# Kernel optimization log

Measured on AMD Instinct MI355X. Metric: run time of the kernel, lower is better.

Reference implementation:

```python
import jax, jax.numpy as jnp
import numpy as np

N_NODES = 100000
N_EDGES = 1600000
IN_FEATS, HIDDEN, N_CLASSES = 128, 64, 16


def setup_inputs() -> dict:
    key = jax.random.key(0)
    ks = jax.random.split(key, 10)
    feats = jax.random.normal(ks[0], (N_NODES, IN_FEATS), dtype=jnp.float32)
    src = jax.random.randint(ks[1], (N_EDGES,), 0, N_NODES, dtype=jnp.int32)
    dst = jax.random.randint(ks[2], (N_EDGES,), 0, N_NODES, dtype=jnp.int32)
    def glorot(k, fan_in, fan_out):
        lim = np.sqrt(6.0 / (fan_in + fan_out)).astype(np.float32)
        return jax.random.uniform(k, (fan_in, fan_out), jnp.float32, -lim, lim)
    return {
        "features": feats, "src": src, "dst": dst,
        "W0": glorot(ks[3], IN_FEATS, HIDDEN), "b0": jnp.zeros((HIDDEN,), jnp.float32),
        "W1": glorot(ks[4], HIDDEN, HIDDEN), "b1": jnp.zeros((HIDDEN,), jnp.float32),
        "W2": glorot(ks[5], HIDDEN, N_CLASSES), "b2": jnp.zeros((N_CLASSES,), jnp.float32),
    }


def _graph_conv(src, dst, x, W, b, act):
    # DGL GraphConv, norm='both': out = D_in^{-1/2} A (D_out^{-1/2} x) W + b
    n = x.shape[0]
    ones = jnp.ones((src.shape[0],), x.dtype)
    deg_out = jnp.clip(jax.ops.segment_sum(ones, src, num_segments=n), 1.0)
    deg_in = jnp.clip(jax.ops.segment_sum(ones, dst, num_segments=n), 1.0)
    # DGL applies W first when in_dim > out_dim (same math, less edge traffic)
    pre = x.shape[1] > W.shape[1]
    h = x @ W if pre else x
    h = h * jax.lax.rsqrt(deg_out)[:, None]
    agg = jax.ops.segment_sum(h[src], dst, num_segments=n)  # [N, d]
    agg = agg * jax.lax.rsqrt(deg_in)[:, None]
    out = (agg if pre else agg @ W) + b
    return act(out) if act is not None else out


def reference(features, src, dst, W0, b0, W1, b1, W2, b2):
    relu = jax.nn.relu
    h = _graph_conv(src, dst, features, W0, b0, relu)
    h = _graph_conv(src, dst, h, W1, b1, relu)        # dropout p=0.0 -> identity
    h = _graph_conv(src, dst, h, W2, b2, None)
    return h
```

## Files before the change

kernel.cpp:

```cpp
#include <hip/hip_runtime.h>

#define NN 100000
#define NE 1600000
#define NBUCK 782
#define PCHUNK 8192
#define HISTB 256
#define NREP 8
#define STAGE_CAP 12288

struct alignas(8) US4 { unsigned short x, y, z, w; };

__device__ __forceinline__ float bfu(unsigned int hw) { return __uint_as_float(hw << 16); }
__device__ __forceinline__ unsigned short f2bf(float f) {
    unsigned int u = __float_as_uint(f);
    return (unsigned short)((u + 0x7fffu + ((u >> 16) & 1u)) >> 16);
}


__global__ __launch_bounds__(256) void k_hist(const int* __restrict__ src,
                                              const int* __restrict__ dst,
                                              int* __restrict__ bcnt8_d,
                                              int* __restrict__ bcnt8_s) {
    __shared__ int hd[NBUCK], hs[NBUCK];
    int tid = threadIdx.x;
    for (int i = tid; i < NBUCK; i += 256) { hd[i] = 0; hs[i] = 0; }
    __syncthreads();
    int* md = bcnt8_d + (size_t)(blockIdx.x & (NREP - 1)) * NBUCK;
    int* ms = bcnt8_s + (size_t)(blockIdx.x & (NREP - 1)) * NBUCK;
    int stride = gridDim.x * 256;
    for (int e = blockIdx.x * 256 + tid; e < NE; e += stride) {
        atomicAdd(&hd[dst[e] >> 7], 1);
        atomicAdd(&hs[src[e] >> 7], 1);
    }
    __syncthreads();
    for (int i = tid; i < NBUCK; i += 256) {
        if (hd[i]) atomicAdd(&md[i], hd[i]);
        if (hs[i]) atomicAdd(&ms[i], hs[i]);
    }
}

__global__ __launch_bounds__(1024) void k_bscan(const int* __restrict__ bcnt8_d,
                                                const int* __restrict__ bcnt8_s,
                                                int* __restrict__ base_d,
                                                int* __restrict__ base_s,
                                                unsigned long long* __restrict__ cur64,
                                                unsigned short* __restrict__ A,
                                                unsigned short* __restrict__ B,
                                                unsigned short* __restrict__ C16,
                                                int* __restrict__ EBg) {
    int t = threadIdx.x;
    if (blockIdx.x == 1) {
        if (t < 64) {
            A[(size_t)NN * 64 + t] = 0;
            B[(size_t)NN * 64 + t] = 0;
        }
        if (t < 16) {
            C16[(size_t)NN * 16 + t] = 0;
            EBg[NE + t] = NN;
        }
        return;
    }
    __shared__ int tmp[1024];
    int v = 0;
    if (t < NBUCK)
#pragma unroll
        for (int c = 0; c < NREP; ++c) v += bcnt8_d[c * NBUCK + t];
    tmp[t] = v;
    __syncthreads();
    for (int off = 1; off < 1024; off <<= 1) {
        int u = (t >= off) ? tmp[t - off] : 0;
        __syncthreads();
        tmp[t] += u;
        __syncthreads();
    }
    int excl_d = tmp[t] - v;
    if (t < NBUCK) base_d[t] = excl_d;
    if (t == 0) base_d[NBUCK] = NE;
    __syncthreads();
    v = 0;
    if (t < NBUCK)
#pragma unroll
        for (int c = 0; c < NREP; ++c) v += bcnt8_s[c * NBUCK + t];
    tmp[t] = v;
    __syncthreads();
    for (int off = 1; off < 1024; off <<= 1) {
        int u = (t >= off) ? tmp[t - off] : 0;
        __syncthreads();
        tmp[t] += u;
        __syncthreads();
    }
    int excl_s = tmp[t] - v;
    if (t < NBUCK) {
        base_s[t] = excl_s;
        cur64[t] = (unsigned long long)(unsigned)excl_d |
                   ((unsigned long long)(unsigned)excl_s << 32);
    }
    if (t == 0) base_s[NBUCK] = NE;
}

__global__ __launch_bounds__(512) void k_pairs(const int* __restrict__ src,
                                               const int* __restrict__ dst,
                                               unsigned long long* __restrict__ cur64,
                                               int* __restrict__ E2d,
                                               unsigned char* __restrict__ E2s) {
    __shared__ int hist_d[NBUCK], gbase_d[NBUCK], hist_s[NBUCK], gbase_s[NBUCK];
    int tid = threadIdx.x;
    for (int i = tid; i < NBUCK; i += 512) { hist_d[i] = 0; hist_s[i] = 0; }
    __syncthreads();
    int base = blockIdx.x * PCHUNK;
#pragma unroll
    for (int i = 0; i < PCHUNK / 512; ++i) {
        int e = base + i * 512 + tid;
        if (e < NE) {
            atomicAdd(&hist_d[dst[e] >> 7], 1);
            atomicAdd(&hist_s[src[e] >> 7], 1);
        }
    }
    __syncthreads();
    int rot = (int)((blockIdx.x * 191u) % NBUCK);
    for (int ii = tid; ii < NBUCK; ii += 512) {
        int i = ii + rot;
        if (i >= NBUCK) i -= NBUCK;
        int hd = hist_d[i], hs = hist_s[i];
        if (hd | hs) {
            unsigned long long r = atomicAdd(
                &cur64[i], (unsigned long long)(unsigned)hd |
                               ((unsigned long long)(unsigned)hs << 32));
            gbase_d[i] = (int)(r & 0xffffffffu);
            gbase_s[i] = (int)(r >> 32);
        }
        hist_d[i] = 0;
        hist_s[i] = 0;
    }
    __syncthreads();
#pragma unroll
    for (int i = 0; i < PCHUNK / 512; ++i) {
        int e = base + i * 512 + tid;
        if (e < NE) {
            int s = src[e], d = dst[e];
            int bd = d >> 7;
            int pd = atomicAdd(&hist_d[bd], 1);
            E2d[gbase_d[bd] + pd] = (s << 7) | (d & 127);
            int bs = s >> 7;
            int ps = atomicAdd(&hist_s[bs], 1);
            E2s[gbase_s[bs] + ps] = (unsigned char)(s & 127);
        }
    }
}

__global__ __launch_bounds__(256) void k_nodes(int* __restrict__ EB,
                                               const int* __restrict__ base_d,
                                               const unsigned char* __restrict__ E2s,
                                               const int* __restrict__ base_s,
                                               int* __restrict__ rowdesc,
                                               float* __restrict__ r_in,
                                               float* __restrict__ r_out) {
    __shared__ int cnt[128], cur[128];
    __shared__ int stage[STAGE_CAP];
    int tid = threadIdx.x;
    int b = blockIdx.x;
    if (b >= NBUCK) {
        b -= NBUCK;
        int base = base_s[b], end = base_s[b + 1];
        if (tid < 128) cnt[tid] = 0;
        __syncthreads();
        for (int i = base + tid; i < end; i += 256) atomicAdd(&cnt[E2s[i]], 1);
        __syncthreads();
        if (tid < 128) {
            int node = b * 128 + tid;
            if (node < NN) r_out[node] = rsqrtf((float)max(cnt[tid], 1));
        }
        return;
    }
    int base = base_d[b], end = base_d[b + 1];
    int m = min(end - base, STAGE_CAP);
    if (tid < 128) cnt[tid] = 0;
    __syncthreads();
    for (int i = tid; i < m; i += 256) {
        int e = EB[base + i];
        stage[i] = e;
        atomicAdd(&cnt[e & 127], 1);
    }
    __syncthreads();
    int v = (tid < 128) ? cnt[tid] : 0;
    for (int off = 1; off < 128; off <<= 1) {
        int u = (tid >= off && tid < 128) ? cnt[tid - off] : 0;
        __syncthreads();
        if (tid < 128) cnt[tid] += u;
        __syncthreads();
    }
    if (tid < 128) {
        int excl = cnt[tid] - v;
        cur[tid] = excl;
        int node = b * 128 + tid;
        if (node < NN) {
            rowdesc[node] = ((base + excl) << 9) | min(v, 511);
            r_in[node] = rsqrtf((float)max(v, 1));
        }
    }
    __syncthreads();
    for (int i = tid; i < m; i += 256) {
        int e = stage[i];
        int pos = atomicAdd(&cur[e & 127], 1);
        EB[base + pos] = e >> 7;
    }
}


__global__ __launch_bounds__(256) void k_gemm0(const float* __restrict__ x,
                                               const float* __restrict__ W0,
                                               const float* __restrict__ r_out,
                                               unsigned short* __restrict__ A) {
    __shared__ float xl[64 * 129];
    __shared__ float wl[64 * 64];
    int tid = threadIdx.x;
    int m0 = blockIdx.x * 64;
#pragma unroll
    for (int i = 0; i < 8; ++i) {
        int idx = i * 256 + tid;
        int m = idx >> 5, kc = idx & 31;
        int gm = min(m0 + m, NN - 1);
        float4 v = *(const float4*)&x[(size_t)gm * 128 + kc * 4];
        float* p = &xl[m * 129 + kc * 4];
        p[0] = v.x; p[1] = v.y; p[2] = v.z; p[3] = v.w;
    }
    int tn = tid & 15, tm = tid >> 4;
    float acc[4][4] = {};
    const float4* W4 = (const float4*)W0;
    float4* wl4 = (float4*)wl;
    for (int h = 0; h < 2; ++h) {
        __syncthreads();
#pragma unroll
        for (int i = 0; i < 4; ++i) wl4[i * 256 + tid] = W4[h * 1024 + i * 256 + tid];
        __syncthreads();
#pragma unroll 4
        for (int k = 0; k < 64; ++k) {
            int kk = h * 64 + k;
            float4 wv = *(const float4*)&wl[k * 64 + tn * 4];
            float xv[4];
#pragma unroll
            for (int i = 0; i < 4; ++i) xv[i] = xl[(tm * 4 + i) * 129 + kk];
#pragma unroll
            for (int i = 0; i < 4; ++i) {
                acc[i][0] = fmaf(xv[i], wv.x, acc[i][0]);
                acc[i][1] = fmaf(xv[i], wv.y, acc[i][1]);
                acc[i][2] = fmaf(xv[i], wv.z, acc[i][2]);
                acc[i][3] = fmaf(xv[i], wv.w, acc[i][3]);
            }
        }
    }
#pragma unroll
    for (int i = 0; i < 4; ++i) {
        int m = m0 + tm * 4 + i;
        if (m < NN) {
            float ro = r_out[m];
            US4 o = {f2bf(acc[i][0] * ro), f2bf(acc[i][1] * ro),
                     f2bf(acc[i][2] * ro), f2bf(acc[i][3] * ro)};
            *(US4*)&A[(size_t)m * 64 + tn * 4] = o;
        }
    }
}

__global__ __launch_bounds__(256) void k_mlp(const unsigned short* __restrict__ G,
                                             const float* __restrict__ W1,
                                             const float* __restrict__ b1,
                                             const float* __restrict__ W2,
                                             const float* __restrict__ r_out,
                                             unsigned short* __restrict__ C16) {
    __shared__ float gl[64 * 65];
    __shared__ float w1l[64 * 64];
    __shared__ float w2l[64 * 16];
    int tid = threadIdx.x;
    int m0 = blockIdx.x * 64;
#pragma unroll
    for (int i = 0; i < 2; ++i) {
        int idx = i * 256 + tid;
        int m = idx >> 3, c8 = idx & 7;
        int gm = min(m0 + m, NN - 1);
        uint4 u = *(const uint4*)&G[(size_t)gm * 64 + c8 * 8];
        float* p = &gl[m * 65 + c8 * 8];
        p[0] = bfu(u.x & 0xffffu); p[1] = bfu(u.x >> 16);
        p[2] = bfu(u.y & 0xffffu); p[3] = bfu(u.y >> 16);
        p[4] = bfu(u.z & 0xffffu); p[5] = bfu(u.z >> 16);
        p[6] = bfu(u.w & 0xffffu); p[7] = bfu(u.w >> 16);
    }
    float4* w1l4 = (float4*)w1l;
    const float4* W1_4 = (const float4*)W1;
#pragma unroll
    for (int i = 0; i < 4; ++i) w1l4[i * 256 + tid] = W1_4[i * 256 + tid];
    ((float4*)w2l)[tid] = ((const float4*)W2)[tid];
    __syncthreads();
    int tn = tid & 15, tm = tid >> 4;
    float acc[4][4] = {};
#pragma unroll 4
    for (int k = 0; k < 64; ++k) {
        float4 wv = *(const float4*)&w1l[k * 64 + tn * 4];
        float xv[4];
#pragma unroll
        for (int i = 0; i < 4; ++i) xv[i] = gl[(tm * 4 + i) * 65 + k];
#pragma unroll
        for (int i = 0; i < 4; ++i) {
            acc[i][0] = fmaf(xv[i], wv.x, acc[i][0]);
            acc[i][1] = fmaf(xv[i], wv.y, acc[i][1]);
            acc[i][2] = fmaf(xv[i], wv.z, acc[i][2]);
            acc[i][3] = fmaf(xv[i], wv.w, acc[i][3]);
        }
    }
    float4 bb = *(const float4*)&b1[tn * 4];
    __syncthreads();
#pragma unroll
    for (int i = 0; i < 4; ++i) {
        gl[(tm * 4 + i) * 65 + tn * 4 + 0] = fmaxf(acc[i][0] + bb.x, 0.f);
        gl[(tm * 4 + i) * 65 + tn * 4 + 1] = fmaxf(acc[i][1] + bb.y, 0.f);
        gl[(tm * 4 + i) * 65 + tn * 4 + 2] = fmaxf(acc[i][2] + bb.z, 0.f);
        gl[(tm * 4 + i) * 65 + tn * 4 + 3] = fmaxf(acc[i][3] + bb.w, 0.f);
    }
    __syncthreads();
    int m = tid >> 2, n0 = (tid & 3) * 4;
    float a2[4] = {};
#pragma unroll 8
    for (int k = 0; k < 64; ++k) {
        float zv = gl[m * 65 + k];
        float4 wv = *(const float4*)&w2l[k * 16 + n0];
        a2[0] = fmaf(zv, wv.x, a2[0]);
        a2[1] = fmaf(zv, wv.y, a2[1]);
        a2[2] = fmaf(zv, wv.z, a2[2]);
        a2[3] = fmaf(zv, wv.w, a2[3]);
    }
    int node = m0 + m;
    if (node < NN) {
        float ro = r_out[node];
        US4 o = {f2bf(a2[0] * ro), f2bf(a2[1] * ro), f2bf(a2[2] * ro), f2bf(a2[3] * ro)};
        *(US4*)&C16[(size_t)node * 16 + n0] = o;
    }
}


template <int MODE>
__global__ __launch_bounds__(256) void k_gb64(const int* __restrict__ rowdesc,
                                              const int* __restrict__ csr,
                                              const unsigned short* __restrict__ h,
                                              const float* __restrict__ r_in,
                                              const float* __restrict__ r_out,
                                              const float* __restrict__ bias,
                                              unsigned short* __restrict__ o16) {
    int tid = threadIdx.x;
    int wave = tid >> 6, lane = tid & 63;
    int n0 = (blockIdx.x * 4 + wave) * 2, n1 = n0 + 1;
    int rdA = rowdesc[n0], rdB = rowdesc[n1];
    int jbA = rdA >> 9, degA = rdA & 511;
    int jbB = rdB >> 9, degB = rdB & 511;
    int itn = max((degA + 7) >> 3, (degB + 7) >> 3);
    int g = lane >> 3, f8 = lane & 7;
    const int* cA = csr + jbA + g;
    const int* cB = csr + jbB + g;
    const unsigned short* hp = h + f8 * 8;
    float aA[8] = {}, aB[8] = {};
    for (int it = 0; it < itn; it += 2) {
        int s0 = it * 8 + g, s1 = s0 + 8;
        int eA0 = cA[it * 8];
        int eA1 = cA[it * 8 + 8];
        int eB0 = cB[it * 8];
        int eB1 = cB[it * 8 + 8];
        eA0 = (s0 < degA) ? eA0 : NN;
        eA1 = (s1 < degA) ? eA1 : NN;
        eB0 = (s0 < degB) ? eB0 : NN;
        eB1 = (s1 < degB) ? eB1 : NN;
        uint4 u0 = *(const uint4*)(hp + (size_t)eA0 * 64);
        uint4 u1 = *(const uint4*)(hp + (size_t)eA1 * 64);
        uint4 u2 = *(const uint4*)(hp + (size_t)eB0 * 64);
        uint4 u3 = *(const uint4*)(hp + (size_t)eB1 * 64);
        aA[0] += bfu(u0.x & 0xffffu); aA[1] += bfu(u0.x >> 16);
        aA[2] += bfu(u0.y & 0xffffu); aA[3] += bfu(u0.y >> 16);
        aA[4] += bfu(u0.z & 0xffffu); aA[5] += bfu(u0.z >> 16);
        aA[6] += bfu(u0.w & 0xffffu); aA[7] += bfu(u0.w >> 16);
        aA[0] += bfu(u1.x & 0xffffu); aA[1] += bfu(u1.x >> 16);
        aA[2] += bfu(u1.y & 0xffffu); aA[3] += bfu(u1.y >> 16);
        aA[4] += bfu(u1.z & 0xffffu); aA[5] += bfu(u1.z >> 16);
        aA[6] += bfu(u1.w & 0xffffu); aA[7] += bfu(u1.w >> 16);
        aB[0] += bfu(u2.x & 0xffffu); aB[1] += bfu(u2.x >> 16);
        aB[2] += bfu(u2.y & 0xffffu); aB[3] += bfu(u2.y >> 16);
        aB[4] += bfu(u2.z & 0xffffu); aB[5] += bfu(u2.z >> 16);
        aB[6] += bfu(u2.w & 0xffffu); aB[7] += bfu(u2.w >> 16);
        aB[0] += bfu(u3.x & 0xffffu); aB[1] += bfu(u3.x >> 16);
        aB[2] += bfu(u3.y & 0xffffu); aB[3] += bfu(u3.y >> 16);
        aB[4] += bfu(u3.z & 0xffffu); aB[5] += bfu(u3.z >> 16);
        aB[6] += bfu(u3.w & 0xffffu); aB[7] += bfu(u3.w >> 16);
    }
#pragma unroll
    for (int m = 8; m <= 32; m <<= 1) {
#pragma unroll
        for (int k = 0; k < 8; ++k) {
            aA[k] += __shfl_xor(aA[k], m);
            aB[k] += __shfl_xor(aB[k], m);
        }
    }
    if (g < 2) {
        int nw = g ? n1 : n0;
        float o[8];
#pragma unroll
        for (int k = 0; k < 8; ++k) o[k] = g ? aB[k] : aA[k];
        float ri = r_in[nw];
        unsigned short ov[8];
        if (MODE == 0) {
            float ro = r_out[nw];
            float4 bA = *(const float4*)&bias[f8 * 8];
            float4 bB = *(const float4*)&bias[f8 * 8 + 4];
            float bb[8] = {bA.x, bA.y, bA.z, bA.w, bB.x, bB.y, bB.z, bB.w};
#pragma unroll
            for (int k = 0; k < 8; ++k)
                ov[k] = f2bf(fmaxf(fmaf(o[k], ri, bb[k]), 0.f) * ro);
        } else {
#pragma unroll
            for (int k = 0; k < 8; ++k) ov[k] = f2bf(o[k] * ri);
        }
        uint4 ow;
        ow.x = (unsigned)ov[0] | ((unsigned)ov[1] << 16);
        ow.y = (unsigned)ov[2] | ((unsigned)ov[3] << 16);
        ow.z = (unsigned)ov[4] | ((unsigned)ov[5] << 16);
        ow.w = (unsigned)ov[6] | ((unsigned)ov[7] << 16);
        *(uint4*)&o16[(size_t)nw * 64 + f8 * 8] = ow;
    }
}

__global__ __launch_bounds__(256) void k_gb16(const int* __restrict__ rowdesc,
                                              const int* __restrict__ csr,
                                              const unsigned short* __restrict__ C16,
                                              const float* __restrict__ r_in,
                                              const float* __restrict__ b2,
                                              float* __restrict__ out) {
    int tid = threadIdx.x;
    int wave = tid >> 6, lane = tid & 63;
    int n0 = (blockIdx.x * 4 + wave) * 2, n1 = n0 + 1;
    int rdA = rowdesc[n0], rdB = rowdesc[n1];
    int jbA = rdA >> 9, degA = rdA & 511;
    int jbB = rdB >> 9, degB = rdB & 511;
    int itn = max((degA + 7) >> 3, (degB + 7) >> 3);
    int g = lane >> 3, p = lane & 7;
    const int* cA = csr + jbA + g;
    const int* cB = csr + jbB + g;
    const unsigned short* cp = C16 + p * 2;
    float a0A = 0.f, a1A = 0.f, a0B = 0.f, a1B = 0.f;
    for (int it = 0; it < itn; it += 2) {
        int s0 = it * 8 + g, s1 = s0 + 8;
        int eA0 = cA[it * 8];
        int eA1 = cA[it * 8 + 8];
        int eB0 = cB[it * 8];
        int eB1 = cB[it * 8 + 8];
        eA0 = (s0 < degA) ? eA0 : NN;
        eA1 = (s1 < degA) ? eA1 : NN;
        eB0 = (s0 < degB) ? eB0 : NN;
        eB1 = (s1 < degB) ? eB1 : NN;
        unsigned u0 = *(const unsigned*)(cp + (size_t)eA0 * 16);
        unsigned u1 = *(const unsigned*)(cp + (size_t)eA1 * 16);
        unsigned u2 = *(const unsigned*)(cp + (size_t)eB0 * 16);
        unsigned u3 = *(const unsigned*)(cp + (size_t)eB1 * 16);
        a0A += bfu(u0 & 0xffffu); a1A += bfu(u0 >> 16);
        a0A += bfu(u1 & 0xffffu); a1A += bfu(u1 >> 16);
        a0B += bfu(u2 & 0xffffu); a1B += bfu(u2 >> 16);
        a0B += bfu(u3 & 0xffffu); a1B += bfu(u3 >> 16);
    }
#pragma unroll
    for (int m = 8; m <= 32; m <<= 1) {
        a0A += __shfl_xor(a0A, m);
        a1A += __shfl_xor(a1A, m);
        a0B += __shfl_xor(a0B, m);
        a1B += __shfl_xor(a1B, m);
    }
    if (g < 2) {
        int nw = g ? n1 : n0;
        float x0 = g ? a0B : a0A;
        float x1 = g ? a1B : a1A;
        float ri = r_in[nw];
        float2 bb = *(const float2*)&b2[p * 2];
        float2 o;
        o.x = fmaf(x0, ri, bb.x);
        o.y = fmaf(x1, ri, bb.y);
        *(float2*)&out[(size_t)nw * 16 + p * 2] = o;
    }
}

extern "C" void kernel_launch(void* const* d_in, const int* in_sizes, int n_in,
                              void* d_out, int out_size, void* d_ws, size_t ws_size,
                              hipStream_t stream) {
    const float* feats = (const float*)d_in[0];
    const int* src = (const int*)d_in[1];
    const int* dst = (const int*)d_in[2];
    const float* W0 = (const float*)d_in[3];
    const float* b0 = (const float*)d_in[4];
    const float* W1 = (const float*)d_in[5];
    const float* b1 = (const float*)d_in[6];
    const float* W2 = (const float*)d_in[7];
    const float* b2 = (const float*)d_in[8];
    float* out = (float*)d_out;

    float* ws = (float*)d_ws;
    float* r_out = ws;
    float* r_in = ws + NN;
    int* rowdesc = (int*)(ws + 2 * NN);
    int* EB = (int*)(ws + 3 * NN);
    unsigned char* E2s = (unsigned char*)(ws + 3 * NN + NE + 16);
    float* R1 = ws + 3 * NN + NE + 16 + NE / 4;
    float* R2 = R1 + (size_t)32 * (NN + 1);
    float* Creg = R2 + (size_t)32 * (NN + 1);
    int* base_d = (int*)(Creg + (size_t)8 * (NN + 1));
    int* base_s = base_d + NBUCK + 1;
    int* cur_raw = base_s + NBUCK + 1;
    unsigned long long* cur64 =
        (unsigned long long*)(cur_raw + (((size_t)(cur_raw - (int*)ws)) & 1));
    int* bcnt8_d = (int*)(cur64 + NBUCK);
    int* bcnt8_s = bcnt8_d + NREP * NBUCK;

    unsigned short* A = (unsigned short*)R1;
    unsigned short* G = A;
    unsigned short* B = (unsigned short*)R2;
    unsigned short* C16 = (unsigned short*)Creg;

    hipMemsetAsync(bcnt8_d, 0, 2 * NREP * NBUCK * sizeof(int), stream);
    k_hist<<<HISTB, 256, 0, stream>>>(src, dst, bcnt8_d, bcnt8_s);
    k_bscan<<<2, 1024, 0, stream>>>(bcnt8_d, bcnt8_s, base_d, base_s, cur64,
                                    A, B, C16, EB);
    k_pairs<<<(NE + PCHUNK - 1) / PCHUNK, 512, 0, stream>>>(src, dst, cur64, EB, E2s);
    k_nodes<<<2 * NBUCK, 256, 0, stream>>>(EB, base_d, E2s, base_s, rowdesc, r_in, r_out);

    k_gemm0<<<(NN + 63) / 64, 256, 0, stream>>>(feats, W0, r_out, A);
    k_gb64<0><<<NN / 8, 256, 0, stream>>>(rowdesc, EB, A, r_in, r_out, b0, B);

    k_gb64<1><<<NN / 8, 256, 0, stream>>>(rowdesc, EB, B, r_in, r_out, b0, G);
    k_mlp<<<(NN + 63) / 64, 256, 0, stream>>>(G, W1, b1, W2, r_out, C16);

    k_gb16<<<NN / 8, 256, 0, stream>>>(rowdesc, EB, C16, r_in, b2, out);
}
```

Baseline: 334.5 us.

## Fuse all graph-conv stages into one persistent kernel with grid barriers

Replaces the chain of separate kernels (histogram, scan, pair scatter, node build, GEMM, three gathers, MLP) with a single persistent kernel of 512 blocks of 512 threads. Stages are separated by a hierarchical software grid barrier that uses atomic counters in workspace. Work in each stage is spread over the fixed grid with grid-stride loops. The aim is to remove per-launch overhead and idle gaps between the many short kernels. In exchange it depends on all blocks being co-resident, loses per-stage launch-shape tuning, and shares one union of shared memory across stages, which could limit occupancy.

```diff
diff --git a/kernel.cpp b/kernel.cpp
--- a/kernel.cpp
+++ b/kernel.cpp
@@ -3,8 +3,10 @@
 #define NN 100000
 #define NE 1600000
 #define NBUCK 782
+#define NB 512
+#define NT 512
 #define PCHUNK 8192
-#define HISTB 256
+#define NPB 196
 #define NREP 8
 #define STAGE_CAP 12288
 
@@ -16,467 +18,479 @@
     return (unsigned short)((u + 0x7fffu + ((u >> 16) & 1u)) >> 16);
 }
 
-
-__global__ __launch_bounds__(256) void k_hist(const int* __restrict__ src,
-                                              const int* __restrict__ dst,
-                                              int* __restrict__ bcnt8_d,
-                                              int* __restrict__ bcnt8_s) {
-    __shared__ int hd[NBUCK], hs[NBUCK];
+__device__ __forceinline__ void gbar(int* bars, int idx) {
+    __syncthreads();
+    if (threadIdx.x == 0) {
+        __threadfence();
+        int* base = bars + idx * 16;
+        int g = (int)(blockIdx.x & 7);
+        if (atomicAdd(&base[g], 1) == (NB / 8) - 1) atomicAdd(&base[8], 1);
+        while (__hip_atomic_load(&base[8], __ATOMIC_RELAXED,
+                                 __HIP_MEMORY_SCOPE_AGENT) < 8) {
+            __builtin_amdgcn_s_sleep(2);
+        }
+        __threadfence();
+    }
+    __syncthreads();
+}
+
+template <int MODE>
+__device__ __forceinline__ void gb64_phase(int bid, int tid,
+                                           const int* __restrict__ rowdesc,
+                                           const int* __restrict__ csr,
+                                           const unsigned short* __restrict__ h,
+                                           const float* __restrict__ r_in,
+                                           const float* __restrict__ r_out,
+                                           const float* __restrict__ bias,
+                                           unsigned short* __restrict__ o16) {
+    int wave = tid >> 6, lane = tid & 63;
+    int g = lane >> 3, f8 = lane & 7;
+    const unsigned short* hp = h + f8 * 8;
+    for (int u = bid; u < NN / 16; u += NB) {
+        int n0 = (u * 8 + wave) * 2, n1 = n0 + 1;
+        int rdA = rowdesc[n0], rdB = rowdesc[n1];
+        int jbA = rdA >> 9, degA = rdA & 511;
+        int jbB = rdB >> 9, degB = rdB & 511;
+        int itn = max((degA + 7) >> 3, (degB + 7) >> 3);
+        const int* cA = csr + jbA + g;
+        const int* cB = csr + jbB + g;
+        float aA[8] = {}, aB[8] = {};
+        for (int it = 0; it < itn; it += 2) {
+            int s0 = it * 8 + g, s1 = s0 + 8;
+            int eA0 = cA[it * 8];
+            int eA1 = cA[it * 8 + 8];
+            int eB0 = cB[it * 8];
+            int eB1 = cB[it * 8 + 8];
+            eA0 = (s0 < degA) ? eA0 : NN;
+            eA1 = (s1 < degA) ? eA1 : NN;
+            eB0 = (s0 < degB) ? eB0 : NN;
+            eB1 = (s1 < degB) ? eB1 : NN;
+            uint4 u0 = *(const uint4*)(hp + (size_t)eA0 * 64);
+            uint4 u1 = *(const uint4*)(hp + (size_t)eA1 * 64);
+            uint4 u2 = *(const uint4*)(hp + (size_t)eB0 * 64);
+            uint4 u3 = *(const uint4*)(hp + (size_t)eB1 * 64);
+            aA[0] += bfu(u0.x & 0xffffu); aA[1] += bfu(u0.x >> 16);
+            aA[2] += bfu(u0.y & 0xffffu); aA[3] += bfu(u0.y >> 16);
+            aA[4] += bfu(u0.z & 0xffffu); aA[5] += bfu(u0.z >> 16);
+            aA[6] += bfu(u0.w & 0xffffu); aA[7] += bfu(u0.w >> 16);
+            aA[0] += bfu(u1.x & 0xffffu); aA[1] += bfu(u1.x >> 16);
+            aA[2] += bfu(u1.y & 0xffffu); aA[3] += bfu(u1.y >> 16);
+            aA[4] += bfu(u1.z & 0xffffu); aA[5] += bfu(u1.z >> 16);
+            aA[6] += bfu(u1.w & 0xffffu); aA[7] += bfu(u1.w >> 16);
+            aB[0] += bfu(u2.x & 0xffffu); aB[1] += bfu(u2.x >> 16);
+            aB[2] += bfu(u2.y & 0xffffu); aB[3] += bfu(u2.y >> 16);
+            aB[4] += bfu(u2.z & 0xffffu); aB[5] += bfu(u2.z >> 16);
+            aB[6] += bfu(u2.w & 0xffffu); aB[7] += bfu(u2.w >> 16);
+            aB[0] += bfu(u3.x & 0xffffu); aB[1] += bfu(u3.x >> 16);
+            aB[2] += bfu(u3.y & 0xffffu); aB[3] += bfu(u3.y >> 16);
+            aB[4] += bfu(u3.z & 0xffffu); aB[5] += bfu(u3.z >> 16);
+            aB[6] += bfu(u3.w & 0xffffu); aB[7] += bfu(u3.w >> 16);
+        }
+#pragma unroll
+        for (int m = 8; m <= 32; m <<= 1) {
+#pragma unroll
+            for (int k = 0; k < 8; ++k) {
+                aA[k] += __shfl_xor(aA[k], m);
+                aB[k] += __shfl_xor(aB[k], m);
+            }
+        }
+        if (g < 2) {
+            int nw = g ? n1 : n0;
+            float o[8];
+#pragma unroll
+            for (int k = 0; k < 8; ++k) o[k] = g ? aB[k] : aA[k];
+            float ri = r_in[nw];
+            unsigned short ov[8];
+            if (MODE == 0) {
+                float ro = r_out[nw];
+                float4 bA = *(const float4*)&bias[f8 * 8];
+                float4 bB = *(const float4*)&bias[f8 * 8 + 4];
+                float bb[8] = {bA.x, bA.y, bA.z, bA.w, bB.x, bB.y, bB.z, bB.w};
+#pragma unroll
+                for (int k = 0; k < 8; ++k)
+                    ov[k] = f2bf(fmaxf(fmaf(o[k], ri, bb[k]), 0.f) * ro);
+            } else {
+#pragma unroll
+                for (int k = 0; k < 8; ++k) ov[k] = f2bf(o[k] * ri);
+            }
+            uint4 ow;
+            ow.x = (unsigned)ov[0] | ((unsigned)ov[1] << 16);
+            ow.y = (unsigned)ov[2] | ((unsigned)ov[3] << 16);
+            ow.z = (unsigned)ov[4] | ((unsigned)ov[5] << 16);
+            ow.w = (unsigned)ov[6] | ((unsigned)ov[7] << 16);
+            *(uint4*)&o16[(size_t)nw * 64 + f8 * 8] = ow;
+        }
+    }
+}
+
+struct SmemT {
+    union {
+        struct { int hd[NBUCK]; int hs[NBUCK]; } hist;
+        struct { int psum[NT]; } scan;
+        struct { int hist_d[NBUCK], gbase_d[NBUCK], hist_s[NBUCK], gbase_s[NBUCK]; } pairs;
+        struct { int cnt[128], cur[128]; int stage[STAGE_CAP]; } nodes;
+        struct { float xl[128 * 65]; float wl[64 * 64]; } gemm;
+        struct { float gl[128 * 65]; float w1l[64 * 64]; float w2l[64 * 16]; } mlp;
+    };
+};
+
+__global__ __launch_bounds__(NT, 4) void k_fused(
+    const float* __restrict__ x, const int* __restrict__ src,
+    const int* __restrict__ dst, const float* __restrict__ W0,
+    const float* __restrict__ b0, const float* __restrict__ W1,
+    const float* __restrict__ b1, const float* __restrict__ W2,
+    const float* __restrict__ b2, float* __restrict__ out,
+    float* __restrict__ r_out, float* __restrict__ r_in,
+    int* __restrict__ rowdesc, int* __restrict__ EB,
+    unsigned char* __restrict__ E2s, int* __restrict__ base_d,
+    int* __restrict__ base_s, unsigned long long* __restrict__ cur64,
+    int* __restrict__ bcnt8_d, int* __restrict__ bcnt8_s,
+    int* __restrict__ bars, unsigned short* __restrict__ A,
+    unsigned short* __restrict__ B, unsigned short* __restrict__ C16) {
+    __shared__ SmemT sm;
     int tid = threadIdx.x;
-    for (int i = tid; i < NBUCK; i += 256) { hd[i] = 0; hs[i] = 0; }
-    __syncthreads();
-    int* md = bcnt8_d + (size_t)(blockIdx.x & (NREP - 1)) * NBUCK;
-    int* ms = bcnt8_s + (size_t)(blockIdx.x & (NREP - 1)) * NBUCK;
-    int stride = gridDim.x * 256;
-    for (int e = blockIdx.x * 256 + tid; e < NE; e += stride) {
-        atomicAdd(&hd[dst[e] >> 7], 1);
-        atomicAdd(&hs[src[e] >> 7], 1);
-    }
-    __syncthreads();
-    for (int i = tid; i < NBUCK; i += 256) {
-        if (hd[i]) atomicAdd(&md[i], hd[i]);
-        if (hs[i]) atomicAdd(&ms[i], hs[i]);
-    }
-}
-
-__global__ __launch_bounds__(1024) void k_bscan(const int* __restrict__ bcnt8_d,
-                                                const int* __restrict__ bcnt8_s,
-                                                int* __restrict__ base_d,
-                                                int* __restrict__ base_s,
-                                                unsigned long long* __restrict__ cur64,
-                                                unsigned short* __restrict__ A,
-                                                unsigned short* __restrict__ B,
-                                                unsigned short* __restrict__ C16,
-                                                int* __restrict__ EBg) {
-    int t = threadIdx.x;
-    if (blockIdx.x == 1) {
-        if (t < 64) {
-            A[(size_t)NN * 64 + t] = 0;
-            B[(size_t)NN * 64 + t] = 0;
-        }
-        if (t < 16) {
-            C16[(size_t)NN * 16 + t] = 0;
-            EBg[NE + t] = NN;
-        }
-        return;
-    }
-    __shared__ int tmp[1024];
-    int v = 0;
-    if (t < NBUCK)
-#pragma unroll
-        for (int c = 0; c < NREP; ++c) v += bcnt8_d[c * NBUCK + t];
-    tmp[t] = v;
-    __syncthreads();
-    for (int off = 1; off < 1024; off <<= 1) {
-        int u = (t >= off) ? tmp[t - off] : 0;
+    int bid = blockIdx.x;
+
+    {
+        int tot = 2 * NREP * NBUCK;
+        for (int i = bid * NT + tid; i < tot; i += NB * NT) bcnt8_d[i] = 0;
+        if (bid == 0) {
+            if (tid < 64) {
+                A[(size_t)NN * 64 + tid] = 0;
+                B[(size_t)NN * 64 + tid] = 0;
+            }
+            if (tid < 16) {
+                C16[(size_t)NN * 16 + tid] = 0;
+                EB[NE + tid] = NN;
+            }
+        }
+    }
+    gbar(bars, 0);
+
+    {
+        for (int i = tid; i < NBUCK; i += NT) { sm.hist.hd[i] = 0; sm.hist.hs[i] = 0; }
         __syncthreads();
-        tmp[t] += u;
+        int* md = bcnt8_d + (size_t)(bid & (NREP - 1)) * NBUCK;
+        int* ms = bcnt8_s + (size_t)(bid & (NREP - 1)) * NBUCK;
+        for (int e = bid * NT + tid; e < NE; e += NB * NT) {
+            atomicAdd(&sm.hist.hd[dst[e] >> 7], 1);
+            atomicAdd(&sm.hist.hs[src[e] >> 7], 1);
+        }
         __syncthreads();
-    }
-    int excl_d = tmp[t] - v;
-    if (t < NBUCK) base_d[t] = excl_d;
-    if (t == 0) base_d[NBUCK] = NE;
-    __syncthreads();
-    v = 0;
-    if (t < NBUCK)
-#pragma unroll
-        for (int c = 0; c < NREP; ++c) v += bcnt8_s[c * NBUCK + t];
-    tmp[t] = v;
-    __syncthreads();
-    for (int off = 1; off < 1024; off <<= 1) {
-        int u = (t >= off) ? tmp[t - off] : 0;
+        for (int i = tid; i < NBUCK; i += NT) {
+            if (sm.hist.hd[i]) atomicAdd(&md[i], sm.hist.hd[i]);
+            if (sm.hist.hs[i]) atomicAdd(&ms[i], sm.hist.hs[i]);
+        }
+    }
+    gbar(bars, 1);
+
+    if (bid == 0) {
+        for (int side = 0; side < 2; ++side) {
+            const int* bc = side ? bcnt8_s : bcnt8_d;
+            int* base = side ? base_s : base_d;
+            int b0i = 2 * tid, b1i = 2 * tid + 1;
+            int s0 = 0, s1 = 0;
+            if (b0i < NBUCK)
+#pragma unroll
+                for (int c = 0; c < NREP; ++c) s0 += bc[c * NBUCK + b0i];
+            if (b1i < NBUCK)
+#pragma unroll
+                for (int c = 0; c < NREP; ++c) s1 += bc[c * NBUCK + b1i];
+            int tot = s0 + s1;
+            sm.scan.psum[tid] = tot;
+            __syncthreads();
+            for (int off = 1; off < NT; off <<= 1) {
+                int u = (tid >= off) ? sm.scan.psum[tid - off] : 0;
+                __syncthreads();
+                sm.scan.psum[tid] += u;
+                __syncthreads();
+            }
+            int excl = sm.scan.psum[tid] - tot;
+            if (b0i < NBUCK) base[b0i] = excl;
+            if (b1i < NBUCK) base[b1i] = excl + s0;
+            if (tid == 0) base[NBUCK] = NE;
+            __syncthreads();
+        }
+        for (int b = tid; b < NBUCK; b += NT)
+            cur64[b] = (unsigned long long)(unsigned)base_d[b] |
+                       ((unsigned long long)(unsigned)base_s[b] << 32);
+    }
+    gbar(bars, 2);
+
+    if (bid < NPB) {
+        for (int i = tid; i < NBUCK; i += NT) { sm.pairs.hist_d[i] = 0; sm.pairs.hist_s[i] = 0; }
         __syncthreads();
-        tmp[t] += u;
+        int base = bid * PCHUNK;
+#pragma unroll
+        for (int i = 0; i < PCHUNK / NT; ++i) {
+            int e = base + i * NT + tid;
+            if (e < NE) {
+                atomicAdd(&sm.pairs.hist_d[dst[e] >> 7], 1);
+                atomicAdd(&sm.pairs.hist_s[src[e] >> 7], 1);
+            }
+        }
         __syncthreads();
-    }
-    int excl_s = tmp[t] - v;
-    if (t < NBUCK) {
-        base_s[t] = excl_s;
-        cur64[t] = (unsigned long long)(unsigned)excl_d |
-                   ((unsigned long long)(unsigned)excl_s << 32);
-    }
-    if (t == 0) base_s[NBUCK] = NE;
-}
-
-__global__ __launch_bounds__(512) void k_pairs(const int* __restrict__ src,
-                                               const int* __restrict__ dst,
-                                               unsigned long long* __restrict__ cur64,
-                                               int* __restrict__ E2d,
-                                               unsigned char* __restrict__ E2s) {
-    __shared__ int hist_d[NBUCK], gbase_d[NBUCK], hist_s[NBUCK], gbase_s[NBUCK];
-    int tid = threadIdx.x;
-    for (int i = tid; i < NBUCK; i += 512) { hist_d[i] = 0; hist_s[i] = 0; }
-    __syncthreads();
-    int base = blockIdx.x * PCHUNK;
-#pragma unroll
-    for (int i = 0; i < PCHUNK / 512; ++i) {
-        int e = base + i * 512 + tid;
-        if (e < NE) {
-            atomicAdd(&hist_d[dst[e] >> 7], 1);
-            atomicAdd(&hist_s[src[e] >> 7], 1);
-        }
-    }
-    __syncthreads();
-    int rot = (int)((blockIdx.x * 191u) % NBUCK);
-    for (int ii = tid; ii < NBUCK; ii += 512) {
-        int i = ii + rot;
-        if (i >= NBUCK) i -= NBUCK;
-        int hd = hist_d[i], hs = hist_s[i];
-        if (hd | hs) {
-            unsigned long long r = atomicAdd(
-                &cur64[i], (unsigned long long)(unsigned)hd |
-                               ((unsigned long long)(unsigned)hs << 32));
-            gbase_d[i] = (int)(r & 0xffffffffu);
-            gbase_s[i] = (int)(r >> 32);
-        }
-        hist_d[i] = 0;
-        hist_s[i] = 0;
-    }
-    __syncthreads();
-#pragma unroll
-    for (int i = 0; i < PCHUNK / 512; ++i) {
-        int e = base + i * 512 + tid;
-        if (e < NE) {
-            int s = src[e], d = dst[e];
-            int bd = d >> 7;
-            int pd = atomicAdd(&hist_d[bd], 1);
-            E2d[gbase_d[bd] + pd] = (s << 7) | (d & 127);
-            int bs = s >> 7;
-            int ps = atomicAdd(&hist_s[bs], 1);
-            E2s[gbase_s[bs] + ps] = (unsigned char)(s & 127);
-        }
-    }
-}
-
-__global__ __launch_bounds__(256) void k_nodes(int* __restrict__ EB,
-                                               const int* __restrict__ base_d,
-                                               const unsigned char* __restrict__ E2s,
-                                               const int* __restrict__ base_s,
-                                               int* __restrict__ rowdesc,
-                                               float* __restrict__ r_in,
-                                               float* __restrict__ r_out) {
-    __shared__ int cnt[128], cur[128];
-    __shared__ int stage[STAGE_CAP];
-    int tid = threadIdx.x;
-    int b = blockIdx.x;
-    if (b >= NBUCK) {
-        b -= NBUCK;
-        int base = base_s[b], end = base_s[b + 1];
-        if (tid < 128) cnt[tid] = 0;
+        int rot = (int)((bid * 191u) % NBUCK);
+        for (int ii = tid; ii < NBUCK; ii += NT) {
+            int i = ii + rot;
+            if (i >= NBUCK) i -= NBUCK;
+            int hd = sm.pairs.hist_d[i], hs = sm.pairs.hist_s[i];
+            if (hd | hs) {
+                unsigned long long r = atomicAdd(
+                    &cur64[i], (unsigned long long)(unsigned)hd |
+                                   ((unsigned long long)(unsigned)hs << 32));
+                sm.pairs.gbase_d[i] = (int)(r & 0xffffffffu);
+                sm.pairs.gbase_s[i] = (int)(r >> 32);
+            }
+            sm.pairs.hist_d[i] = 0;
+            sm.pairs.hist_s[i] = 0;
+        }
         __syncthreads();
-        for (int i = base + tid; i < end; i += 256) atomicAdd(&cnt[E2s[i]], 1);
+#pragma unroll
+        for (int i = 0; i < PCHUNK / NT; ++i) {
+            int e = base + i * NT + tid;
+            if (e < NE) {
+                int s = src[e], d = dst[e];
+                int bd = d >> 7;
+                int pd = atomicAdd(&sm.pairs.hist_d[bd], 1);
+                EB[sm.pairs.gbase_d[bd] + pd] = (s << 7) | (d & 127);
+                int bs = s >> 7;
+                int ps = atomicAdd(&sm.pairs.hist_s[bs], 1);
+                E2s[sm.pairs.gbase_s[bs] + ps] = (unsigned char)(s & 127);
+            }
+        }
+    }
+    gbar(bars, 3);
+
+    for (int bb = bid; bb < 2 * NBUCK; bb += NB) {
         __syncthreads();
-        if (tid < 128) {
-            int node = b * 128 + tid;
-            if (node < NN) r_out[node] = rsqrtf((float)max(cnt[tid], 1));
-        }
-        return;
-    }
-    int base = base_d[b], end = base_d[b + 1];
-    int m = min(end - base, STAGE_CAP);
-    if (tid < 128) cnt[tid] = 0;
-    __syncthreads();
-    for (int i = tid; i < m; i += 256) {
-        int e = EB[base + i];
-        stage[i] = e;
-        atomicAdd(&cnt[e & 127], 1);
-    }
-    __syncthreads();
-    int v = (tid < 128) ? cnt[tid] : 0;
-    for (int off = 1; off < 128; off <<= 1) {
-        int u = (tid >= off && tid < 128) ? cnt[tid - off] : 0;
-        __syncthreads();
-        if (tid < 128) cnt[tid] += u;
-        __syncthreads();
-    }
-    if (tid < 128) {
-        int excl = cnt[tid] - v;
-        cur[tid] = excl;
-        int node = b * 128 + tid;
-        if (node < NN) {
-            rowdesc[node] = ((base + excl) << 9) | min(v, 511);
-            r_in[node] = rsqrtf((float)max(v, 1));
-        }
-    }
-    __syncthreads();
-    for (int i = tid; i < m; i += 256) {
-        int e = stage[i];
-        int pos = atomicAdd(&cur[e & 127], 1);
-        EB[base + pos] = e >> 7;
-    }
-}
-
-
-__global__ __launch_bounds__(256) void k_gemm0(const float* __restrict__ x,
-                                               const float* __restrict__ W0,
-                                               const float* __restrict__ r_out,
-                                               unsigned short* __restrict__ A) {
-    __shared__ float xl[64 * 129];
-    __shared__ float wl[64 * 64];
-    int tid = threadIdx.x;
-    int m0 = blockIdx.x * 64;
-#pragma unroll
-    for (int i = 0; i < 8; ++i) {
-        int idx = i * 256 + tid;
-        int m = idx >> 5, kc = idx & 31;
-        int gm = min(m0 + m, NN - 1);
-        float4 v = *(const float4*)&x[(size_t)gm * 128 + kc * 4];
-        float* p = &xl[m * 129 + kc * 4];
-        p[0] = v.x; p[1] = v.y; p[2] = v.z; p[3] = v.w;
-    }
-    int tn = tid & 15, tm = tid >> 4;
-    float acc[4][4] = {};
-    const float4* W4 = (const float4*)W0;
-    float4* wl4 = (float4*)wl;
-    for (int h = 0; h < 2; ++h) {
-        __syncthreads();
-#pragma unroll
-        for (int i = 0; i < 4; ++i) wl4[i * 256 + tid] = W4[h * 1024 + i * 256 + tid];
-        __syncthreads();
+        if (bb >= NBUCK) {
+            int b = bb - NBUCK;
+            int base = base_s[b], end = base_s[b + 1];
+            if (tid < 128) sm.nodes.cnt[tid] = 0;
+            __syncthreads();
+            for (int i = base + tid; i < end; i += NT) atomicAdd(&sm.nodes.cnt[E2s[i]], 1);
+            __syncthreads();
+            if (tid < 128) {
+                int node = b * 128 + tid;
+                if (node < NN) r_out[node] = rsqrtf((float)max(sm.nodes.cnt[tid], 1));
+            }
+        } else {
+            int b = bb;
+            int base = base_d[b], end = base_d[b + 1];
+            int m = min(end - base, STAGE_CAP);
+            if (tid < 128) sm.nodes.cnt[tid] = 0;
+            __syncthreads();
+            for (int i = tid; i < m; i += NT) {
+                int e = EB[base + i];
+                sm.nodes.stage[i] = e;
+                atomicAdd(&sm.nodes.cnt[e & 127], 1);
+            }
+            __syncthreads();
+            int v = (tid < 128) ? sm.nodes.cnt[tid] : 0;
+            for (int off = 1; off < 128; off <<= 1) {
+                int u = (tid >= off && tid < 128) ? sm.nodes.cnt[tid - off] : 0;
+                __syncthreads();
+                if (tid < 128) sm.nodes.cnt[tid] += u;
+                __syncthreads();
+            }
+            if (tid < 128) {
+                int excl = sm.nodes.cnt[tid] - v;
+                sm.nodes.cur[tid] = excl;
+                int node = b * 128 + tid;
+                if (node < NN) {
+                    rowdesc[node] = ((base + excl) << 9) | min(v, 511);
+                    r_in[node] = rsqrtf((float)max(v, 1));
+                }
+            }
+            __syncthreads();
+            for (int i = tid; i < m; i += NT) {
+                int e = sm.nodes.stage[i];
+                int pos = atomicAdd(&sm.nodes.cur[e & 127], 1);
+                EB[base + pos] = e >> 7;
+            }
+        }
+    }
+    gbar(bars, 4);
+
+    {
+        int tn = tid & 15, tm = tid >> 4;
+        const float4* W4 = (const float4*)W0;
+        float4* wl4 = (float4*)sm.gemm.wl;
+        for (int tile = bid; tile < (NN + 127) / 128; tile += NB) {
+            int m0 = tile * 128;
+            float acc[4][4] = {};
+            for (int h = 0; h < 2; ++h) {
+                __syncthreads();
+#pragma unroll
+                for (int i = 0; i < 4; ++i) {
+                    int idx = i * NT + tid;
+                    int m = idx >> 4, kc = idx & 15;
+                    int gm = min(m0 + m, NN - 1);
+                    float4 v = *(const float4*)&x[(size_t)gm * 128 + h * 64 + kc * 4];
+                    float* p = &sm.gemm.xl[m * 65 + kc * 4];
+                    p[0] = v.x; p[1] = v.y; p[2] = v.z; p[3] = v.w;
+                }
+#pragma unroll
+                for (int i = 0; i < 2; ++i) wl4[i * NT + tid] = W4[h * 1024 + i * NT + tid];
+                __syncthreads();
 #pragma unroll 4
-        for (int k = 0; k < 64; ++k) {
-            int kk = h * 64 + k;
-            float4 wv = *(const float4*)&wl[k * 64 + tn * 4];
-            float xv[4];
-#pragma unroll
-            for (int i = 0; i < 4; ++i) xv[i] = xl[(tm * 4 + i) * 129 + kk];
+                for (int k = 0; k < 64; ++k) {
+                    float4 wv = *(const float4*)&sm.gemm.wl[k * 64 + tn * 4];
+                    float xv[4];
+#pragma unroll
+                    for (int i = 0; i < 4; ++i) xv[i] = sm.gemm.xl[(tm * 4 + i) * 65 + k];
+#pragma unroll
+                    for (int i = 0; i < 4; ++i) {
+                        acc[i][0] = fmaf(xv[i], wv.x, acc[i][0]);
+                        acc[i][1] = fmaf(xv[i], wv.y, acc[i][1]);
+                        acc[i][2] = fmaf(xv[i], wv.z, acc[i][2]);
+                        acc[i][3] = fmaf(xv[i], wv.w, acc[i][3]);
+                    }
+                }
+            }
 #pragma unroll
             for (int i = 0; i < 4; ++i) {
-                acc[i][0] = fmaf(xv[i], wv.x, acc[i][0]);
-                acc[i][1] = fmaf(xv[i], wv.y, acc[i][1]);
-                acc[i][2] = fmaf(xv[i], wv.z, acc[i][2]);
-                acc[i][3] = fmaf(xv[i], wv.w, acc[i][3]);
-            }
-        }
-    }
-#pragma unroll
-    for (int i = 0; i < 4; ++i) {
-        int m = m0 + tm * 4 + i;
-        if (m < NN) {
-            float ro = r_out[m];
-            US4 o = {f2bf(acc[i][0] * ro), f2bf(acc[i][1] * ro),
-                     f2bf(acc[i][2] * ro), f2bf(acc[i][3] * ro)};
-            *(US4*)&A[(size_t)m * 64 + tn * 4] = o;
-        }
-    }
-}
-
-__global__ __launch_bounds__(256) void k_mlp(const unsigned short* __restrict__ G,
-                                             const float* __restrict__ W1,
-                                             const float* __restrict__ b1,
-                                             const float* __restrict__ W2,
-                                             const float* __restrict__ r_out,
-                                             unsigned short* __restrict__ C16) {
-    __shared__ float gl[64 * 65];
-    __shared__ float w1l[64 * 64];
-    __shared__ float w2l[64 * 16];
-    int tid = threadIdx.x;
-    int m0 = blockIdx.x * 64;
-#pragma unroll
-    for (int i = 0; i < 2; ++i) {
-        int idx = i * 256 + tid;
-        int m = idx >> 3, c8 = idx & 7;
-        int gm = min(m0 + m, NN - 1);
-        uint4 u = *(const uint4*)&G[(size_t)gm * 64 + c8 * 8];
-        float* p = &gl[m * 65 + c8 * 8];
-        p[0] = bfu(u.x & 0xffffu); p[1] = bfu(u.x >> 16);
-        p[2] = bfu(u.y & 0xffffu); p[3] = bfu(u.y >> 16);
-        p[4] = bfu(u.z & 0xffffu); p[5] = bfu(u.z >> 16);
-        p[6] = bfu(u.w & 0xffffu); p[7] = bfu(u.w >> 16);
-    }
-    float4* w1l4 = (float4*)w1l;
-    const float4* W1_4 = (const float4*)W1;
-#pragma unroll
-    for (int i = 0; i < 4; ++i) w1l4[i * 256 + tid] = W1_4[i * 256 + tid];
-    ((float4*)w2l)[tid] = ((const float4*)W2)[tid];
-    __syncthreads();
-    int tn = tid & 15, tm = tid >> 4;
-    float acc[4][4] = {};
+                int m = m0 + tm * 4 + i;
+                if (m < NN) {
+                    float ro = r_out[m];
+                    US4 o = {f2bf(acc[i][0] * ro), f2bf(acc[i][1] * ro),
+                             f2bf(acc[i][2] * ro), f2bf(acc[i][3] * ro)};
+                    *(US4*)&A[(size_t)m * 64 + tn * 4] = o;
+                }
+            }
+        }
+    }
+    gbar(bars, 5);
+
+    gb64_phase<0>(bid, tid, rowdesc, EB, A, r_in, r_out, b0, B);
+    gbar(bars, 6);
+
+    gb64_phase<1>(bid, tid, rowdesc, EB, B, r_in, r_out, b0, A);
+    gbar(bars, 7);
+
+    {
+        const unsigned short* G = A;
+        int tn = tid & 15, tm = tid >> 4;
+        float4* w1l4 = (float4*)sm.mlp.w1l;
+        const float4* W1_4 = (const float4*)W1;
+        for (int tile = bid; tile < (NN + 127) / 128; tile += NB) {
+            int m0 = tile * 128;
+            __syncthreads();
+#pragma unroll
+            for (int i = 0; i < 2; ++i) {
+                int idx = i * NT + tid;
+                int m = idx >> 3, c8 = idx & 7;
+                int gm = min(m0 + m, NN - 1);
+                uint4 u = *(const uint4*)&G[(size_t)gm * 64 + c8 * 8];
+                float* p = &sm.mlp.gl[m * 65 + c8 * 8];
+                p[0] = bfu(u.x & 0xffffu); p[1] = bfu(u.x >> 16);
+                p[2] = bfu(u.y & 0xffffu); p[3] = bfu(u.y >> 16);
+                p[4] = bfu(u.z & 0xffffu); p[5] = bfu(u.z >> 16);
+                p[6] = bfu(u.w & 0xffffu); p[7] = bfu(u.w >> 16);
+            }
+#pragma unroll
+            for (int i = 0; i < 2; ++i) w1l4[i * NT + tid] = W1_4[i * NT + tid];
+            if (tid < 256) ((float4*)sm.mlp.w2l)[tid] = ((const float4*)W2)[tid];
+            __syncthreads();
+            float acc[4][4] = {};
 #pragma unroll 4
-    for (int k = 0; k < 64; ++k) {
-        float4 wv = *(const float4*)&w1l[k * 64 + tn * 4];
-        float xv[4];
-#pragma unroll
-        for (int i = 0; i < 4; ++i) xv[i] = gl[(tm * 4 + i) * 65 + k];
-#pragma unroll
-        for (int i = 0; i < 4; ++i) {
-            acc[i][0] = fmaf(xv[i], wv.x, acc[i][0]);
-            acc[i][1] = fmaf(xv[i], wv.y, acc[i][1]);
-            acc[i][2] = fmaf(xv[i], wv.z, acc[i][2]);
-            acc[i][3] = fmaf(xv[i], wv.w, acc[i][3]);
-        }
-    }
-    float4 bb = *(const float4*)&b1[tn * 4];
-    __syncthreads();
-#pragma unroll
-    for (int i = 0; i < 4; ++i) {
-        gl[(tm * 4 + i) * 65 + tn * 4 + 0] = fmaxf(acc[i][0] + bb.x, 0.f);
-        gl[(tm * 4 + i) * 65 + tn * 4 + 1] = fmaxf(acc[i][1] + bb.y, 0.f);
-        gl[(tm * 4 + i) * 65 + tn * 4 + 2] = fmaxf(acc[i][2] + bb.z, 0.f);
-        gl[(tm * 4 + i) * 65 + tn * 4 + 3] = fmaxf(acc[i][3] + bb.w, 0.f);
-    }
-    __syncthreads();
-    int m = tid >> 2, n0 = (tid & 3) * 4;
-    float a2[4] = {};
+            for (int k = 0; k < 64; ++k) {
+                float4 wv = *(const float4*)&sm.mlp.w1l[k * 64 + tn * 4];
+                float xv[4];
+#pragma unroll
+                for (int i = 0; i < 4; ++i) xv[i] = sm.mlp.gl[(tm * 4 + i) * 65 + k];
+#pragma unroll
+                for (int i = 0; i < 4; ++i) {
+                    acc[i][0] = fmaf(xv[i], wv.x, acc[i][0]);
+                    acc[i][1] = fmaf(xv[i], wv.y, acc[i][1]);
+                    acc[i][2] = fmaf(xv[i], wv.z, acc[i][2]);
+                    acc[i][3] = fmaf(xv[i], wv.w, acc[i][3]);
+                }
+            }
+            float4 bb = *(const float4*)&b1[tn * 4];
+            __syncthreads();
+#pragma unroll
+            for (int i = 0; i < 4; ++i) {
+                sm.mlp.gl[(tm * 4 + i) * 65 + tn * 4 + 0] = fmaxf(acc[i][0] + bb.x, 0.f);
+                sm.mlp.gl[(tm * 4 + i) * 65 + tn * 4 + 1] = fmaxf(acc[i][1] + bb.y, 0.f);
+                sm.mlp.gl[(tm * 4 + i) * 65 + tn * 4 + 2] = fmaxf(acc[i][2] + bb.z, 0.f);
+                sm.mlp.gl[(tm * 4 + i) * 65 + tn * 4 + 3] = fmaxf(acc[i][3] + bb.w, 0.f);
+            }
+            __syncthreads();
+            int m = tid >> 2, n0c = (tid & 3) * 4;
+            float a2[4] = {};
 #pragma unroll 8
-    for (int k = 0; k < 64; ++k) {
-        float zv = gl[m * 65 + k];
-        float4 wv = *(const float4*)&w2l[k * 16 + n0];
-        a2[0] = fmaf(zv, wv.x, a2[0]);
-        a2[1] = fmaf(zv, wv.y, a2[1]);
-        a2[2] = fmaf(zv, wv.z, a2[2]);
-        a2[3] = fmaf(zv, wv.w, a2[3]);
-    }
-    int node = m0 + m;
-    if (node < NN) {
-        float ro = r_out[node];
-        US4 o = {f2bf(a2[0] * ro), f2bf(a2[1] * ro), f2bf(a2[2] * ro), f2bf(a2[3] * ro)};
-        *(US4*)&C16[(size_t)node * 16 + n0] = o;
-    }
-}
-
-
-template <int MODE>
-__global__ __launch_bounds__(256) void k_gb64(const int* __restrict__ rowdesc,
-                                              const int* __restrict__ csr,
-                                              const unsigned short* __restrict__ h,
-                                              const float* __restrict__ r_in,
-                                              const float* __restrict__ r_out,
-                                              const float* __restrict__ bias,
-                                              unsigned short* __restrict__ o16) {
-    int tid = threadIdx.x;
-    int wave = tid >> 6, lane = tid & 63;
-    int n0 = (blockIdx.x * 4 + wave) * 2, n1 = n0 + 1;
-    int rdA = rowdesc[n0], rdB = rowdesc[n1];
-    int jbA = rdA >> 9, degA = rdA & 511;
-    int jbB = rdB >> 9, degB = rdB & 511;
-    int itn = max((degA + 7) >> 3, (degB + 7) >> 3);
-    int g = lane >> 3, f8 = lane & 7;
-    const int* cA = csr + jbA + g;
-    const int* cB = csr + jbB + g;
-    const unsigned short* hp = h + f8 * 8;
-    float aA[8] = {}, aB[8] = {};
-    for (int it = 0; it < itn; it += 2) {
-        int s0 = it * 8 + g, s1 = s0 + 8;
-        int eA0 = cA[it * 8];
-        int eA1 = cA[it * 8 + 8];
-        int eB0 = cB[it * 8];
-        int eB1 = cB[it * 8 + 8];
-        eA0 = (s0 < degA) ? eA0 : NN;
-        eA1 = (s1 < degA) ? eA1 : NN;
-        eB0 = (s0 < degB) ? eB0 : NN;
-        eB1 = (s1 < degB) ? eB1 : NN;
-        uint4 u0 = *(const uint4*)(hp + (size_t)eA0 * 64);
-        uint4 u1 = *(const uint4*)(hp + (size_t)eA1 * 64);
-        uint4 u2 = *(const uint4*)(hp + (size_t)eB0 * 64);
-        uint4 u3 = *(const uint4*)(hp + (size_t)eB1 * 64);
-        aA[0] += bfu(u0.x & 0xffffu); aA[1] += bfu(u0.x >> 16);
-        aA[2] += bfu(u0.y & 0xffffu); aA[3] += bfu(u0.y >> 16);
-        aA[4] += bfu(u0.z & 0xffffu); aA[5] += bfu(u0.z >> 16);
-        aA[6] += bfu(u0.w & 0xffffu); aA[7] += bfu(u0.w >> 16);
-        aA[0] += bfu(u1.x & 0xffffu); aA[1] += bfu(u1.x >> 16);
-        aA[2] += bfu(u1.y & 0xffffu); aA[3] += bfu(u1.y >> 16);
-        aA[4] += bfu(u1.z & 0xffffu); aA[5] += bfu(u1.z >> 16);
-        aA[6] += bfu(u1.w & 0xffffu); aA[7] += bfu(u1.w >> 16);
-        aB[0] += bfu(u2.x & 0xffffu); aB[1] += bfu(u2.x >> 16);
-        aB[2] += bfu(u2.y & 0xffffu); aB[3] += bfu(u2.y >> 16);
-        aB[4] += bfu(u2.z & 0xffffu); aB[5] += bfu(u2.z >> 16);
-        aB[6] += bfu(u2.w & 0xffffu); aB[7] += bfu(u2.w >> 16);
-        aB[0] += bfu(u3.x & 0xffffu); aB[1] += bfu(u3.x >> 16);
-        aB[2] += bfu(u3.y & 0xffffu); aB[3] += bfu(u3.y >> 16);
-        aB[4] += bfu(u3.z & 0xffffu); aB[5] += bfu(u3.z >> 16);
-        aB[6] += bfu(u3.w & 0xffffu); aB[7] += bfu(u3.w >> 16);
-    }
-#pragma unroll
-    for (int m = 8; m <= 32; m <<= 1) {
-#pragma unroll
-        for (int k = 0; k < 8; ++k) {
-            aA[k] += __shfl_xor(aA[k], m);
-            aB[k] += __shfl_xor(aB[k], m);
-        }
-    }
-    if (g < 2) {
-        int nw = g ? n1 : n0;
-        float o[8];
-#pragma unroll
-        for (int k = 0; k < 8; ++k) o[k] = g ? aB[k] : aA[k];
-        float ri = r_in[nw];
-        unsigned short ov[8];
-        if (MODE == 0) {
-            float ro = r_out[nw];
-            float4 bA = *(const float4*)&bias[f8 * 8];
-            float4 bB = *(const float4*)&bias[f8 * 8 + 4];
-            float bb[8] = {bA.x, bA.y, bA.z, bA.w, bB.x, bB.y, bB.z, bB.w};
-#pragma unroll
-            for (int k = 0; k < 8; ++k)
-                ov[k] = f2bf(fmaxf(fmaf(o[k], ri, bb[k]), 0.f) * ro);
-        } else {
-#pragma unroll
-            for (int k = 0; k < 8; ++k) ov[k] = f2bf(o[k] * ri);
-        }
-        uint4 ow;
-        ow.x = (unsigned)ov[0] | ((unsigned)ov[1] << 16);
-        ow.y = (unsigned)ov[2] | ((unsigned)ov[3] << 16);
-        ow.z = (unsigned)ov[4] | ((unsigned)ov[5] << 16);
-        ow.w = (unsigned)ov[6] | ((unsigned)ov[7] << 16);
-        *(uint4*)&o16[(size_t)nw * 64 + f8 * 8] = ow;
-    }
-}
-
-__global__ __launch_bounds__(256) void k_gb16(const int* __restrict__ rowdesc,
-                                              const int* __restrict__ csr,
-                                              const unsigned short* __restrict__ C16,
-                                              const float* __restrict__ r_in,
-                                              const float* __restrict__ b2,
-                                              float* __restrict__ out) {
-    int tid = threadIdx.x;
-    int wave = tid >> 6, lane = tid & 63;
-    int n0 = (blockIdx.x * 4 + wave) * 2, n1 = n0 + 1;
-    int rdA = rowdesc[n0], rdB = rowdesc[n1];
-    int jbA = rdA >> 9, degA = rdA & 511;
-    int jbB = rdB >> 9, degB = rdB & 511;
-    int itn = max((degA + 7) >> 3, (degB + 7) >> 3);
-    int g = lane >> 3, p = lane & 7;
-    const int* cA = csr + jbA + g;
-    const int* cB = csr + jbB + g;
-    const unsigned short* cp = C16 + p * 2;
-    float a0A = 0.f, a1A = 0.f, a0B = 0.f, a1B = 0.f;
-    for (int it = 0; it < itn; it += 2) {
-        int s0 = it * 8 + g, s1 = s0 + 8;
-        int eA0 = cA[it * 8];
-        int eA1 = cA[it * 8 + 8];
-        int eB0 = cB[it * 8];
-        int eB1 = cB[it * 8 + 8];
-        eA0 = (s0 < degA) ? eA0 : NN;
-        eA1 = (s1 < degA) ? eA1 : NN;
-        eB0 = (s0 < degB) ? eB0 : NN;
-        eB1 = (s1 < degB) ? eB1 : NN;
-        unsigned u0 = *(const unsigned*)(cp + (size_t)eA0 * 16);
-        unsigned u1 = *(const unsigned*)(cp + (size_t)eA1 * 16);
-        unsigned u2 = *(const unsigned*)(cp + (size_t)eB0 * 16);
-        unsigned u3 = *(const unsigned*)(cp + (size_t)eB1 * 16);
-        a0A += bfu(u0 & 0xffffu); a1A += bfu(u0 >> 16);
-        a0A += bfu(u1 & 0xffffu); a1A += bfu(u1 >> 16);
-        a0B += bfu(u2 & 0xffffu); a1B += bfu(u2 >> 16);
-        a0B += bfu(u3 & 0xffffu); a1B += bfu(u3 >> 16);
-    }
-#pragma unroll
-    for (int m = 8; m <= 32; m <<= 1) {
-        a0A += __shfl_xor(a0A, m);
-        a1A += __shfl_xor(a1A, m);
-        a0B += __shfl_xor(a0B, m);
-        a1B += __shfl_xor(a1B, m);
-    }
-    if (g < 2) {
-        int nw = g ? n1 : n0;
-        float x0 = g ? a0B : a0A;
-        float x1 = g ? a1B : a1A;
-        float ri = r_in[nw];
-        float2 bb = *(const float2*)&b2[p * 2];
-        float2 o;
-        o.x = fmaf(x0, ri, bb.x);
-        o.y = fmaf(x1, ri, bb.y);
-        *(float2*)&out[(size_t)nw * 16 + p * 2] = o;
+            for (int k = 0; k < 64; ++k) {
+                float zv = sm.mlp.gl[m * 65 + k];
+                float4 wv = *(const float4*)&sm.mlp.w2l[k * 16 + n0c];
+                a2[0] = fmaf(zv, wv.x, a2[0]);
+                a2[1] = fmaf(zv, wv.y, a2[1]);
+                a2[2] = fmaf(zv, wv.z, a2[2]);
+                a2[3] = fmaf(zv, wv.w, a2[3]);
+            }
+            int node = m0 + m;
+            if (node < NN) {
+                float ro = r_out[node];
+                US4 o = {f2bf(a2[0] * ro), f2bf(a2[1] * ro), f2bf(a2[2] * ro),
+                         f2bf(a2[3] * ro)};
+                *(US4*)&C16[(size_t)node * 16 + n0c] = o;
+            }
+        }
+    }
+    gbar(bars, 8);
+
+    {
+        int wave = tid >> 6, lane = tid & 63;
+        int g = lane >> 3, p = lane & 7;
+        const unsigned short* cp = C16 + p * 2;
+        for (int u = bid; u < NN / 16; u += NB) {
+            int n0 = (u * 8 + wave) * 2, n1 = n0 + 1;
+            int rdA = rowdesc[n0], rdB = rowdesc[n1];
+            int jbA = rdA >> 9, degA = rdA & 511;
+            int jbB = rdB >> 9, degB = rdB & 511;
+            int itn = max((degA + 7) >> 3, (degB + 7) >> 3);
+            const int* cA = EB + jbA + g;
+            const int* cB = EB + jbB + g;
+            float a0A = 0.f, a1A = 0.f, a0B = 0.f, a1B = 0.f;
+            for (int it = 0; it < itn; it += 2) {
+                int s0 = it * 8 + g, s1 = s0 + 8;
+                int eA0 = cA[it * 8];
+                int eA1 = cA[it * 8 + 8];
+                int eB0 = cB[it * 8];
+                int eB1 = cB[it * 8 + 8];
+                eA0 = (s0 < degA) ? eA0 : NN;
+                eA1 = (s1 < degA) ? eA1 : NN;
+                eB0 = (s0 < degB) ? eB0 : NN;
+                eB1 = (s1 < degB) ? eB1 : NN;
+                unsigned u0 = *(const unsigned*)(cp + (size_t)eA0 * 16);
+                unsigned u1 = *(const unsigned*)(cp + (size_t)eA1 * 16);
+                unsigned u2 = *(const unsigned*)(cp + (size_t)eB0 * 16);
+                unsigned u3 = *(const unsigned*)(cp + (size_t)eB1 * 16);
+                a0A += bfu(u0 & 0xffffu); a1A += bfu(u0 >> 16);
+                a0A += bfu(u1 & 0xffffu); a1A += bfu(u1 >> 16);
+                a0B += bfu(u2 & 0xffffu); a1B += bfu(u2 >> 16);
+                a0B += bfu(u3 & 0xffffu); a1B += bfu(u3 >> 16);
+            }
+#pragma unroll
+            for (int m = 8; m <= 32; m <<= 1) {
+                a0A += __shfl_xor(a0A, m);
+                a1A += __shfl_xor(a1A, m);
+                a0B += __shfl_xor(a0B, m);
+                a1B += __shfl_xor(a1B, m);
+            }
+            if (g < 2) {
+                int nw = g ? n1 : n0;
+                float x0 = g ? a0B : a0A;
+                float x1 = g ? a1B : a1A;
+                float ri = r_in[nw];
+                float2 bb = *(const float2*)&b2[p * 2];
+                float2 o;
+                o.x = fmaf(x0, ri, bb.x);
+                o.y = fmaf(x1, ri, bb.y);
+                *(float2*)&out[(size_t)nw * 16 + p * 2] = o;
+            }
+        }
     }
 }
 
@@ -510,24 +524,14 @@
         (unsigned long long*)(cur_raw + (((size_t)(cur_raw - (int*)ws)) & 1));
     int* bcnt8_d = (int*)(cur64 + NBUCK);
     int* bcnt8_s = bcnt8_d + NREP * NBUCK;
+    int* bars = bcnt8_s + NREP * NBUCK;
 
     unsigned short* A = (unsigned short*)R1;
-    unsigned short* G = A;
     unsigned short* B = (unsigned short*)R2;
     unsigned short* C16 = (unsigned short*)Creg;
 
-    hipMemsetAsync(bcnt8_d, 0, 2 * NREP * NBUCK * sizeof(int), stream);
-    k_hist<<<HISTB, 256, 0, stream>>>(src, dst, bcnt8_d, bcnt8_s);
-    k_bscan<<<2, 1024, 0, stream>>>(bcnt8_d, bcnt8_s, base_d, base_s, cur64,
-                                    A, B, C16, EB);
-    k_pairs<<<(NE + PCHUNK - 1) / PCHUNK, 512, 0, stream>>>(src, dst, cur64, EB, E2s);
-    k_nodes<<<2 * NBUCK, 256, 0, stream>>>(EB, base_d, E2s, base_s, rowdesc, r_in, r_out);
-
-    k_gemm0<<<(NN + 63) / 64, 256, 0, stream>>>(feats, W0, r_out, A);
-    k_gb64<0><<<NN / 8, 256, 0, stream>>>(rowdesc, EB, A, r_in, r_out, b0, B);
-
-    k_gb64<1><<<NN / 8, 256, 0, stream>>>(rowdesc, EB, B, r_in, r_out, b0, G);
-    k_mlp<<<(NN + 63) / 64, 256, 0, stream>>>(G, W1, b1, W2, r_out, C16);
-
-    k_gb16<<<NN / 8, 256, 0, stream>>>(rowdesc, EB, C16, r_in, b2, out);
+    hipMemsetAsync(bars, 0, 9 * 16 * sizeof(int), stream);
+    k_fused<<<NB, NT, 0, stream>>>(feats, src, dst, W0, b0, W1, b1, W2, b2, out,
+                                   r_out, r_in, rowdesc, EB, E2s, base_d, base_s,
+                                   cur64, bcnt8_d, bcnt8_s, bars, A, B, C16);
 }
```

New measurement: 792.1 us. 2.37x slower.
